# Performance work log

Hardware: AMD Instinct MI355X
Metric: run time of the kernel (lower is better)

The kernel has to match this reference:

```python
import jax, jax.numpy as jnp
import numpy as np

B, S, D, H = 16, 2048, 128, 4
HD = D // H  # 32
EPS = 1e-5


def layer_norm(x, g, b):
    m = jnp.mean(x, axis=-1, keepdims=True)
    v = jnp.mean((x - m) ** 2, axis=-1, keepdims=True)
    return (x - m) * jax.lax.rsqrt(v + EPS) * g + b


def setup_inputs() -> dict:
    key = jax.random.key(0)
    ks = jax.random.split(key, 9)
    lin = lambda k: jax.random.normal(k, (D, D), dtype=jnp.float32) * 0.01  # [in, out]
    return {
        "input0": jax.random.normal(ks[0], (B, S, D), dtype=jnp.float32),
        "Wq": lin(ks[1]), "bq": jnp.zeros((D,), jnp.float32),
        "Wk": lin(ks[2]), "bk": jnp.zeros((D,), jnp.float32),
        "Wv": lin(ks[3]), "bv": jnp.zeros((D,), jnp.float32),
        "Wo": lin(ks[4]), "bo": jnp.zeros((D,), jnp.float32),
        "g1": jnp.ones((D,), jnp.float32), "b1": jnp.zeros((D,), jnp.float32),
        "W1": lin(ks[5]), "bf1": jnp.zeros((D,), jnp.float32),
        "W2": lin(ks[6]), "bf2": jnp.zeros((D,), jnp.float32),
        "g2": jnp.ones((D,), jnp.float32), "b2": jnp.zeros((D,), jnp.float32),
    }


def reference(input0, Wq, bq, Wk, bk, Wv, bv, Wo, bo, g1, b1, W1, bf1, W2, bf2, g2, b2):
    x = input0
    # multi-head attention (self-attention), dropout in eval mode (identity)
    q = (x @ Wq + bq).reshape(B, S, H, HD)
    k = (x @ Wk + bk).reshape(B, S, H, HD)
    v = (x @ Wv + bv).reshape(B, S, H, HD)
    scores = jnp.einsum("bqhd,bkhd->bhqk", q, k) / jnp.sqrt(jnp.float32(HD))
    weights = jax.nn.softmax(scores, axis=-1)
    attn = jnp.einsum("bhqk,bkhd->bqhd", weights, v).reshape(B, S, D)
    attn = attn @ Wo + bo
    attended = layer_norm(attn + x, g1, b1)
    # feed-forward; note residual uses x (not attended), faithful to source
    ff = jax.nn.relu(attended @ W1 + bf1) @ W2 + bf2
    return layer_norm(ff + x, g2, b2)
```

## Files before the change

### kernel.cpp

```cpp
#include <hip/hip_runtime.h>
#include <math.h>

#define NB   16
#define NS   2048
#define ND   128
#define NH   4
#define NHD  32
#define NROWS (NB * NS)

typedef unsigned short u16;
typedef __bf16 bf16x8 __attribute__((ext_vector_type(8)));
typedef float  f32x4  __attribute__((ext_vector_type(4)));
typedef float  f32x16 __attribute__((ext_vector_type(16)));

static __device__ __forceinline__ u16 f2bf(float a) {
    union { __bf16 h; u16 u; } t; t.h = (__bf16)a; return t.u;
}
static __device__ __forceinline__ unsigned int pk2(float a, float b) {
    union { __bf16 h[2]; unsigned int u; } t;
    t.h[0] = (__bf16)a; t.h[1] = (__bf16)b; return t.u;
}

#if __has_builtin(__builtin_amdgcn_exp2f)
#define EXP2(x) __builtin_amdgcn_exp2f(x)
#else
extern "C" __device__ float __ocml_native_exp2_f32(float);
#define EXP2(x) __ocml_native_exp2_f32(x)
#endif

#define QSCALE (0.17677669529663687f * 1.4426950408889634f)

__global__ __launch_bounds__(256) void prep_kernel(
    const float* __restrict__ Wq, const float* __restrict__ Wk,
    const float* __restrict__ Wv, const float* __restrict__ Wo,
    const float* __restrict__ W1, const float* __restrict__ W2,
    u16* __restrict__ wt)
{
    const int wb = blockIdx.x, tid = threadIdx.x;
    const int widx = wb >> 3, sub = wb & 7;
    const float* W = widx == 0 ? Wq : widx == 1 ? Wk : widx == 2 ? Wv
                   : widx == 3 ? Wo : widx == 4 ? W1 : W2;
    const int flat8 = sub * 256 + tid;
    const int n = flat8 >> 4, k0 = (flat8 & 15) * 8;
    float v[8];
    #pragma unroll
    for (int j = 0; j < 8; ++j) v[j] = W[(size_t)(k0 + j) * ND + n];
    int4 o;
    o.x = pk2(v[0], v[1]); o.y = pk2(v[2], v[3]);
    o.z = pk2(v[4], v[5]); o.w = pk2(v[6], v[7]);
    *reinterpret_cast<int4*>(wt + (size_t)widx * 16384 + (size_t)n * ND + k0) = o;
}

__global__ __launch_bounds__(256) void qkv_mfma_kernel(
    const float* __restrict__ x,
    const u16* __restrict__ wtq, const u16* __restrict__ wtk, const u16* __restrict__ wtv,
    const float* __restrict__ bq, const float* __restrict__ bk, const float* __restrict__ bv,
    u16* __restrict__ qo, u16* __restrict__ kfo, u16* __restrict__ vfo)
{
    const int tid = threadIdx.x, lane = tid & 63, w = tid >> 6;
    const int n = lane & 15, c = lane >> 4;
    const int row0 = blockIdx.x * 64;
    const int grow = row0 + w * 16;

    bf16x8 a[4];
    #pragma unroll
    for (int kk = 0; kk < 4; ++kk) {
        const float* xp = x + (size_t)(grow + n) * ND + kk * 32 + c * 8;
        float4 f0 = *reinterpret_cast<const float4*>(xp);
        float4 f1 = *reinterpret_cast<const float4*>(xp + 4);
        union { unsigned int u[4]; bf16x8 v; } t;
        t.u[0] = pk2(f0.x, f0.y); t.u[1] = pk2(f0.z, f0.w);
        t.u[2] = pk2(f1.x, f1.y); t.u[3] = pk2(f1.z, f1.w);
        a[kk] = t.v;
    }

    f32x4 accq[8], acck[8], accv[8];
    #pragma unroll
    for (int nb = 0; nb < 8; ++nb) {
        accq[nb] = f32x4{0.f, 0.f, 0.f, 0.f};
        acck[nb] = f32x4{0.f, 0.f, 0.f, 0.f};
        accv[nb] = f32x4{0.f, 0.f, 0.f, 0.f};
    }

    #pragma unroll
    for (int kk = 0; kk < 4; ++kk) {
        #pragma unroll
        for (int nb = 0; nb < 8; ++nb) {
            const size_t boff = (size_t)(nb * 16 + n) * ND + kk * 32 + c * 8;
            bf16x8 bqf = *reinterpret_cast<const bf16x8*>(wtq + boff);
            bf16x8 bkf = *reinterpret_cast<const bf16x8*>(wtk + boff);
            bf16x8 bvf = *reinterpret_cast<const bf16x8*>(wtv + boff);
            accq[nb] = __builtin_amdgcn_mfma_f32_16x16x32_bf16(a[kk], bqf, accq[nb], 0, 0, 0);
            acck[nb] = __builtin_amdgcn_mfma_f32_16x16x32_bf16(a[kk], bkf, acck[nb], 0, 0, 0);
            accv[nb] = __builtin_amdgcn_mfma_f32_16x16x32_bf16(a[kk], bvf, accv[nb], 0, 0, 0);
        }
    }

    const int b   = row0 >> 11;
    const int sp0 = (row0 & (NS - 1)) + w * 16;

    #pragma unroll
    for (int nb = 0; nb < 8; ++nb) {
        const int col = nb * 16 + n, hh = col >> 5, d32 = col & 31;
        const float bqv = bq[col], bkv = bk[col], bvv = bv[col];
        const size_t kvb = ((size_t)b * NH + hh) * (NS * NHD);

        #pragma unroll
        for (int r = 0; r < 4; ++r)
            qo[kvb + (size_t)(sp0 + 4 * c + r) * NHD + d32] =
                f2bf((accq[nb][r] + bqv) * QSCALE);

        const int s = d32 >> 4, c2 = (d32 >> 3) & 1, j = d32 & 7;
        #pragma unroll
        for (int r = 0; r < 4; ++r) {
            const int key = sp0 + 4 * c + r;
            const int T = key >> 5, l5 = key & 31;
            kfo[kvb + (size_t)(T * 2 + s) * 512 + (size_t)(l5 + 32 * c2) * 8 + j] =
                f2bf(acck[nb][r] + bkv);
        }

        const int lanep = d32 + 32 * (c & 1);
        const int j0    = 4 * (c >> 1);
        float v0 = accv[nb][0] + bvv, v1 = accv[nb][1] + bvv;
        float v2 = accv[nb][2] + bvv, v3 = accv[nb][3] + bvv;
        *reinterpret_cast<uint2*>(
            vfo + kvb + (size_t)(sp0 >> 4) * 512 + (size_t)lanep * 8 + j0) =
            make_uint2(pk2(v0, v1), pk2(v2, v3));
    }
}

__global__ __launch_bounds__(256) void attn_mfma_kernel(
    const u16* __restrict__ qg,
    const u16* __restrict__ kfg,
    const u16* __restrict__ vfg,
    u16* __restrict__ ao)
{
    __shared__ float Ol[2][64][17];
    __shared__ float Dl[2][64];

    const int tid = threadIdx.x, lane = tid & 63, w = tid >> 6;
    const int qhalf = w >> 1, khalf = w & 1;
    const int bh = blockIdx.y, b = bh >> 2, h = bh & 3;
    const int n = lane & 31, hf = lane >> 5;
    const size_t fbase = (size_t)bh * (NS * NHD);
    const int q0w = blockIdx.x * 64 + qhalf * 32;

    const bf16x8 qf0 = *reinterpret_cast<const bf16x8*>(
        qg + fbase + (size_t)(q0w + n) * NHD + 8 * hf);
    const bf16x8 qf1 = *reinterpret_cast<const bf16x8*>(
        qg + fbase + (size_t)(q0w + n) * NHD + 16 + 8 * hf);

    f32x16 ot, zz;
    #pragma unroll
    for (int i = 0; i < 16; ++i) { ot[i] = 0.f; zz[i] = 0.f; }
    float lp = 0.f;

    const u16* kf = kfg + fbase + (size_t)lane * 8 + (size_t)khalf * (16 * 4) * 512;
    const u16* vf = vfg + fbase + (size_t)lane * 8 + (size_t)khalf * (16 * 4) * 512;

    for (int t = 0; t < 16; ++t) {
        const bf16x8 ka00 = *reinterpret_cast<const bf16x8*>(kf + (size_t)(4 * t + 0) * 512);
        const bf16x8 ka01 = *reinterpret_cast<const bf16x8*>(kf + (size_t)(4 * t + 1) * 512);
        const bf16x8 ka10 = *reinterpret_cast<const bf16x8*>(kf + (size_t)(4 * t + 2) * 512);
        const bf16x8 ka11 = *reinterpret_cast<const bf16x8*>(kf + (size_t)(4 * t + 3) * 512);
        const bf16x8 va0  = *reinterpret_cast<const bf16x8*>(vf + (size_t)(4 * t + 0) * 512);
        const bf16x8 va1  = *reinterpret_cast<const bf16x8*>(vf + (size_t)(4 * t + 1) * 512);
        const bf16x8 va2  = *reinterpret_cast<const bf16x8*>(vf + (size_t)(4 * t + 2) * 512);
        const bf16x8 va3  = *reinterpret_cast<const bf16x8*>(vf + (size_t)(4 * t + 3) * 512);

        f32x16 s0 = __builtin_amdgcn_mfma_f32_32x32x16_bf16(ka00, qf0, zz, 0, 0, 0);
        s0 = __builtin_amdgcn_mfma_f32_32x32x16_bf16(ka01, qf1, s0, 0, 0, 0);
        f32x16 s1 = __builtin_amdgcn_mfma_f32_32x32x16_bf16(ka10, qf0, zz, 0, 0, 0);
        s1 = __builtin_amdgcn_mfma_f32_32x32x16_bf16(ka11, qf1, s1, 0, 0, 0);

        {
            float p[16];
            #pragma unroll
            for (int r = 0; r < 16; ++r) p[r] = EXP2(s0[r]);
            float t0 = (p[0] + p[1]) + (p[2] + p[3]);
            float t1 = (p[4] + p[5]) + (p[6] + p[7]);
            float t2 = (p[8] + p[9]) + (p[10] + p[11]);
            float t3 = (p[12] + p[13]) + (p[14] + p[15]);
            lp += (t0 + t1) + (t2 + t3);
            union { unsigned int u[4]; bf16x8 v; } pw0, pw1;
            #pragma unroll
            for (int i = 0; i < 4; ++i) pw0.u[i] = pk2(p[2 * i], p[2 * i + 1]);
            #pragma unroll
            for (int i = 0; i < 4; ++i) pw1.u[i] = pk2(p[8 + 2 * i], p[9 + 2 * i]);
            ot = __builtin_amdgcn_mfma_f32_32x32x16_bf16(va0, pw0.v, ot, 0, 0, 0);
            ot = __builtin_amdgcn_mfma_f32_32x32x16_bf16(va1, pw1.v, ot, 0, 0, 0);
        }
        {
            float p[16];
            #pragma unroll
            for (int r = 0; r < 16; ++r) p[r] = EXP2(s1[r]);
            float t0 = (p[0] + p[1]) + (p[2] + p[3]);
            float t1 = (p[4] + p[5]) + (p[6] + p[7]);
            float t2 = (p[8] + p[9]) + (p[10] + p[11]);
            float t3 = (p[12] + p[13]) + (p[14] + p[15]);
            lp += (t0 + t1) + (t2 + t3);
            union { unsigned int u[4]; bf16x8 v; } pw0, pw1;
            #pragma unroll
            for (int i = 0; i < 4; ++i) pw0.u[i] = pk2(p[2 * i], p[2 * i + 1]);
            #pragma unroll
            for (int i = 0; i < 4; ++i) pw1.u[i] = pk2(p[8 + 2 * i], p[9 + 2 * i]);
            ot = __builtin_amdgcn_mfma_f32_32x32x16_bf16(va2, pw0.v, ot, 0, 0, 0);
            ot = __builtin_amdgcn_mfma_f32_32x32x16_bf16(va3, pw1.v, ot, 0, 0, 0);
        }
    }

    float lpt = lp + __shfl_xor(lp, 32);

    if (khalf) {
        #pragma unroll
        for (int i = 0; i < 16; ++i) Ol[qhalf][lane][i] = ot[i];
        Dl[qhalf][lane] = lpt;
    }
    __syncthreads();
    if (!khalf) {
        #pragma unroll
        for (int i = 0; i < 16; ++i) ot[i] += Ol[qhalf][lane][i];
        const float dn  = lpt + Dl[qhalf][lane];
        const float inv = 1.0f / dn;

        u16* orow = ao + ((size_t)b * NS + q0w + n) * ND + h * NHD + 4 * hf;
        #pragma unroll
        for (int g = 0; g < 4; ++g) {
            uint2 wv = make_uint2(pk2(ot[4 * g] * inv, ot[4 * g + 1] * inv),
                                  pk2(ot[4 * g + 2] * inv, ot[4 * g + 3] * inv));
            *reinterpret_cast<uint2*>(orow + 8 * g) = wv;
        }
    }
}

__global__ __launch_bounds__(256) void tail_kernel(
    const u16* __restrict__ A0, const u16* __restrict__ wto,
    const u16* __restrict__ wt1, const u16* __restrict__ wt2,
    const float* __restrict__ bo, const float* __restrict__ bf1,
    const float* __restrict__ bf2, const float* __restrict__ x,
    const float* __restrict__ g1, const float* __restrict__ b1,
    const float* __restrict__ g2, const float* __restrict__ b2,
    float* __restrict__ outp)
{
    __shared__ __align__(16) u16 tile[64][136];
    const int tid = threadIdx.x, lane = tid & 63, w = tid >> 6;
    const int n = lane & 15, c = lane >> 4;
    const int row0 = blockIdx.x * 64;
    const int grow = row0 + w * 16;
    const int lrow = w * 16;

    bf16x8 a[4];
    f32x4 acc[8];

    #pragma unroll
    for (int kk = 0; kk < 4; ++kk)
        a[kk] = *reinterpret_cast<const bf16x8*>(
            A0 + (size_t)(grow + n) * ND + kk * 32 + c * 8);
    #pragma unroll
    for (int nb = 0; nb < 8; ++nb) acc[nb] = f32x4{0.f, 0.f, 0.f, 0.f};
    #pragma unroll
    for (int kk = 0; kk < 4; ++kk)
        #pragma unroll
        for (int nb = 0; nb < 8; ++nb) {
            bf16x8 bw = *reinterpret_cast<const bf16x8*>(
                wto + (size_t)(nb * 16 + n) * ND + kk * 32 + c * 8);
            acc[nb] = __builtin_amdgcn_mfma_f32_16x16x32_bf16(a[kk], bw, acc[nb], 0, 0, 0);
        }

    {
        float vals[8][4];
        float sr[4]  = {0.f, 0.f, 0.f, 0.f};
        float sr2[4] = {0.f, 0.f, 0.f, 0.f};
        #pragma unroll
        for (int nb = 0; nb < 8; ++nb) {
            const int col = nb * 16 + n;
            const float bb = bo[col];
            #pragma unroll
            for (int r = 0; r < 4; ++r) {
                float vv = acc[nb][r] + bb +
                           x[(size_t)(grow + 4 * c + r) * ND + col];
                vals[nb][r] = vv;
                sr[r]  += vv;
                sr2[r] += vv * vv;
            }
        }
        #pragma unroll
        for (int m = 1; m < 16; m <<= 1)
            #pragma unroll
            for (int r = 0; r < 4; ++r) {
                sr[r]  += __shfl_xor(sr[r],  m);
                sr2[r] += __shfl_xor(sr2[r], m);
            }
        #pragma unroll
        for (int r = 0; r < 4; ++r) {
            float mean = sr[r] * (1.f / 128.f);
            float var  = fmaf(-mean, mean, sr2[r] * (1.f / 128.f));
            float rstd = rsqrtf(var + 1e-5f);
            #pragma unroll
            for (int nb = 0; nb < 8; ++nb) {
                const int col = nb * 16 + n;
                float y = fmaf((vals[nb][r] - mean) * rstd, g1[col], b1[col]);
                tile[lrow + 4 * c + r][col] = f2bf(y);
            }
        }
    }
    __syncthreads();

    #pragma unroll
    for (int kk = 0; kk < 4; ++kk)
        a[kk] = *reinterpret_cast<const bf16x8*>(&tile[lrow + n][kk * 32 + c * 8]);
    __syncthreads();
    #pragma unroll
    for (int nb = 0; nb < 8; ++nb) acc[nb] = f32x4{0.f, 0.f, 0.f, 0.f};
    #pragma unroll
    for (int kk = 0; kk < 4; ++kk)
        #pragma unroll
        for (int nb = 0; nb < 8; ++nb) {
            bf16x8 bw = *reinterpret_cast<const bf16x8*>(
                wt1 + (size_t)(nb * 16 + n) * ND + kk * 32 + c * 8);
            acc[nb] = __builtin_amdgcn_mfma_f32_16x16x32_bf16(a[kk], bw, acc[nb], 0, 0, 0);
        }
    #pragma unroll
    for (int nb = 0; nb < 8; ++nb) {
        const int col = nb * 16 + n;
        const float bb = bf1[col];
        #pragma unroll
        for (int r = 0; r < 4; ++r)
            tile[lrow + 4 * c + r][col] = f2bf(fmaxf(acc[nb][r] + bb, 0.f));
    }
    __syncthreads();

    #pragma unroll
    for (int kk = 0; kk < 4; ++kk)
        a[kk] = *reinterpret_cast<const bf16x8*>(&tile[lrow + n][kk * 32 + c * 8]);
    #pragma unroll
    for (int nb = 0; nb < 8; ++nb) acc[nb] = f32x4{0.f, 0.f, 0.f, 0.f};
    #pragma unroll
    for (int kk = 0; kk < 4; ++kk)
        #pragma unroll
        for (int nb = 0; nb < 8; ++nb) {
            bf16x8 bw = *reinterpret_cast<const bf16x8*>(
                wt2 + (size_t)(nb * 16 + n) * ND + kk * 32 + c * 8);
            acc[nb] = __builtin_amdgcn_mfma_f32_16x16x32_bf16(a[kk], bw, acc[nb], 0, 0, 0);
        }
    {
        float vals[8][4];
        float sr[4]  = {0.f, 0.f, 0.f, 0.f};
        float sr2[4] = {0.f, 0.f, 0.f, 0.f};
        #pragma unroll
        for (int nb = 0; nb < 8; ++nb) {
            const int col = nb * 16 + n;
            const float bb = bf2[col];
            #pragma unroll
            for (int r = 0; r < 4; ++r) {
                float vv = acc[nb][r] + bb +
                           x[(size_t)(grow + 4 * c + r) * ND + col];
                vals[nb][r] = vv;
                sr[r]  += vv;
                sr2[r] += vv * vv;
            }
        }
        #pragma unroll
        for (int m = 1; m < 16; m <<= 1)
            #pragma unroll
            for (int r = 0; r < 4; ++r) {
                sr[r]  += __shfl_xor(sr[r],  m);
                sr2[r] += __shfl_xor(sr2[r], m);
            }
        #pragma unroll
        for (int r = 0; r < 4; ++r) {
            float mean = sr[r] * (1.f / 128.f);
            float var  = fmaf(-mean, mean, sr2[r] * (1.f / 128.f));
            float rstd = rsqrtf(var + 1e-5f);
            #pragma unroll
            for (int nb = 0; nb < 8; ++nb) {
                const int col = nb * 16 + n;
                float y = fmaf((vals[nb][r] - mean) * rstd, g2[col], b2[col]);
                outp[(size_t)(grow + 4 * c + r) * ND + col] = y;
            }
        }
    }
}

extern "C" void kernel_launch(void* const* d_in, const int* in_sizes, int n_in,
                              void* d_out, int out_size, void* d_ws, size_t ws_size,
                              hipStream_t stream)
{
    const float* x   = (const float*)d_in[0];
    const float* Wq  = (const float*)d_in[1];
    const float* bq  = (const float*)d_in[2];
    const float* Wk  = (const float*)d_in[3];
    const float* bk  = (const float*)d_in[4];
    const float* Wv  = (const float*)d_in[5];
    const float* bv  = (const float*)d_in[6];
    const float* Wo  = (const float*)d_in[7];
    const float* bo  = (const float*)d_in[8];
    const float* g1  = (const float*)d_in[9];
    const float* b1  = (const float*)d_in[10];
    const float* W1  = (const float*)d_in[11];
    const float* bf1 = (const float*)d_in[12];
    const float* W2  = (const float*)d_in[13];
    const float* bf2 = (const float*)d_in[14];
    const float* g2  = (const float*)d_in[15];
    const float* b2  = (const float*)d_in[16];
    float* outp = (float*)d_out;

    const size_t NE = (size_t)NROWS * ND;
    u16* wt  = (u16*)d_ws;
    u16* qb  = wt + 6 * 16384;
    u16* kfb = qb + NE;
    u16* vfb = kfb + NE;
    u16* aob = vfb + NE;

    dim3 blk(256);
    prep_kernel<<<dim3(48), blk, 0, stream>>>(Wq, Wk, Wv, Wo, W1, W2, wt);
    qkv_mfma_kernel<<<dim3(NROWS / 64), blk, 0, stream>>>(
        x, wt + 0 * 16384, wt + 1 * 16384, wt + 2 * 16384, bq, bk, bv, qb, kfb, vfb);
    attn_mfma_kernel<<<dim3(NS / 64, NB * NH), blk, 0, stream>>>(qb, kfb, vfb, aob);
    tail_kernel<<<dim3(NROWS / 64), blk, 0, stream>>>(
        aob, wt + 3 * 16384, wt + 4 * 16384, wt + 5 * 16384,
        bo, bf1, bf2, x, g1, b1, g2, b2, outp);
}
```

Baseline: 129.6 us.

## Stage K through LDS, transpose Q layout, and software-pipeline attention loop

The QKV kernel now writes Q in a d-major (transposed) layout with packed 8-byte stores. K is staged through a shared-memory tile so it can be written to its fragment layout with 16-byte stores instead of scattered 2-byte stores. The attention kernel uses a 1D grid with a block-id swizzle that groups batch-heads, and restructures the key loop into 32 single-tile iterations that prefetch the next K/V fragments and raise wave priority around the MFMAs. Costs include strided 2-byte gathers to load Q in attention, an extra barrier in the QKV kernel, and a changed L2 access order.

```diff
diff --git a/kernel.cpp b/kernel.cpp
--- a/kernel.cpp
+++ b/kernel.cpp
@@ -55,8 +55,10 @@
     const float* __restrict__ x,
     const u16* __restrict__ wtq, const u16* __restrict__ wtk, const u16* __restrict__ wtv,
     const float* __restrict__ bq, const float* __restrict__ bk, const float* __restrict__ bv,
-    u16* __restrict__ qo, u16* __restrict__ kfo, u16* __restrict__ vfo)
+    u16* __restrict__ qdm, u16* __restrict__ kfo, u16* __restrict__ vfo)
 {
+    __shared__ __align__(16) u16 tileK[64][136];
+
     const int tid = threadIdx.x, lane = tid & 63, w = tid >> 6;
     const int n = lane & 15, c = lane >> 4;
     const int row0 = blockIdx.x * 64;
@@ -96,8 +98,9 @@
         }
     }
 
-    const int b   = row0 >> 11;
-    const int sp0 = (row0 & (NS - 1)) + w * 16;
+    const int b    = row0 >> 11;
+    const int sp0b = row0 & (NS - 1);
+    const int sp0  = sp0b + w * 16;
 
     #pragma unroll
     for (int nb = 0; nb < 8; ++nb) {
@@ -105,19 +108,16 @@
         const float bqv = bq[col], bkv = bk[col], bvv = bv[col];
         const size_t kvb = ((size_t)b * NH + hh) * (NS * NHD);
 
+        float q0 = (accq[nb][0] + bqv) * QSCALE;
+        float q1 = (accq[nb][1] + bqv) * QSCALE;
+        float q2 = (accq[nb][2] + bqv) * QSCALE;
+        float q3 = (accq[nb][3] + bqv) * QSCALE;
+        *reinterpret_cast<uint2*>(qdm + kvb + (size_t)d32 * NS + sp0 + 4 * c) =
+            make_uint2(pk2(q0, q1), pk2(q2, q3));
+
         #pragma unroll
         for (int r = 0; r < 4; ++r)
-            qo[kvb + (size_t)(sp0 + 4 * c + r) * NHD + d32] =
-                f2bf((accq[nb][r] + bqv) * QSCALE);
-
-        const int s = d32 >> 4, c2 = (d32 >> 3) & 1, j = d32 & 7;
-        #pragma unroll
-        for (int r = 0; r < 4; ++r) {
-            const int key = sp0 + 4 * c + r;
-            const int T = key >> 5, l5 = key & 31;
-            kfo[kvb + (size_t)(T * 2 + s) * 512 + (size_t)(l5 + 32 * c2) * 8 + j] =
-                f2bf(acck[nb][r] + bkv);
-        }
+            tileK[w * 16 + 4 * c + r][col] = f2bf(acck[nb][r] + bkv);
 
         const int lanep = d32 + 32 * (c & 1);
         const int j0    = 4 * (c >> 1);
@@ -127,10 +127,29 @@
             vfo + kvb + (size_t)(sp0 >> 4) * 512 + (size_t)lanep * 8 + j0) =
             make_uint2(pk2(v0, v1), pk2(v2, v3));
     }
+
+    __syncthreads();
+
+    {
+        const int lk = w * 16 + (lane >> 2);
+        const int gk = sp0b + lk;
+        const int T = gk >> 5, l5 = gk & 31;
+        #pragma unroll
+        for (int i = 0; i < 4; ++i) {
+            const int m16  = (lane & 3) + 4 * i;
+            const int col0 = m16 * 8;
+            const int hh = col0 >> 5, d32 = col0 & 31;
+            const int s = d32 >> 4, c2 = (d32 >> 3) & 1;
+            const size_t kvb = ((size_t)b * NH + hh) * (NS * NHD);
+            int4 vv = *reinterpret_cast<const int4*>(&tileK[lk][col0]);
+            *reinterpret_cast<int4*>(
+                kfo + kvb + (size_t)(T * 2 + s) * 512 + (size_t)(l5 + 32 * c2) * 8) = vv;
+        }
+    }
 }
 
 __global__ __launch_bounds__(256) void attn_mfma_kernel(
-    const u16* __restrict__ qg,
+    const u16* __restrict__ qdm,
     const u16* __restrict__ kfg,
     const u16* __restrict__ vfg,
     u16* __restrict__ ao)
@@ -140,75 +159,71 @@
 
     const int tid = threadIdx.x, lane = tid & 63, w = tid >> 6;
     const int qhalf = w >> 1, khalf = w & 1;
-    const int bh = blockIdx.y, b = bh >> 2, h = bh & 3;
+
+    const int bid  = blockIdx.x;
+    const int bh   = (bid & 7) * 8 + ((bid >> 3) & 7);
+    const int qblk = bid >> 6;
+    const int b = bh >> 2, h = bh & 3;
     const int n = lane & 31, hf = lane >> 5;
     const size_t fbase = (size_t)bh * (NS * NHD);
-    const int q0w = blockIdx.x * 64 + qhalf * 32;
-
-    const bf16x8 qf0 = *reinterpret_cast<const bf16x8*>(
-        qg + fbase + (size_t)(q0w + n) * NHD + 8 * hf);
-    const bf16x8 qf1 = *reinterpret_cast<const bf16x8*>(
-        qg + fbase + (size_t)(q0w + n) * NHD + 16 + 8 * hf);
+    const int q0w = qblk * 64 + qhalf * 32;
+
+    union { u16 h[8]; bf16x8 v; } q0u, q1u;
+    {
+        const u16* qb = qdm + fbase + (q0w + n);
+        #pragma unroll
+        for (int i = 0; i < 8; ++i) {
+            q0u.h[i] = qb[(size_t)(8 * hf + i) * NS];
+            q1u.h[i] = qb[(size_t)(16 + 8 * hf + i) * NS];
+        }
+    }
+    const bf16x8 qf0 = q0u.v, qf1 = q1u.v;
 
     f32x16 ot, zz;
     #pragma unroll
     for (int i = 0; i < 16; ++i) { ot[i] = 0.f; zz[i] = 0.f; }
-    float lp = 0.f;
-
-    const u16* kf = kfg + fbase + (size_t)lane * 8 + (size_t)khalf * (16 * 4) * 512;
-    const u16* vf = vfg + fbase + (size_t)lane * 8 + (size_t)khalf * (16 * 4) * 512;
-
-    for (int t = 0; t < 16; ++t) {
-        const bf16x8 ka00 = *reinterpret_cast<const bf16x8*>(kf + (size_t)(4 * t + 0) * 512);
-        const bf16x8 ka01 = *reinterpret_cast<const bf16x8*>(kf + (size_t)(4 * t + 1) * 512);
-        const bf16x8 ka10 = *reinterpret_cast<const bf16x8*>(kf + (size_t)(4 * t + 2) * 512);
-        const bf16x8 ka11 = *reinterpret_cast<const bf16x8*>(kf + (size_t)(4 * t + 3) * 512);
-        const bf16x8 va0  = *reinterpret_cast<const bf16x8*>(vf + (size_t)(4 * t + 0) * 512);
-        const bf16x8 va1  = *reinterpret_cast<const bf16x8*>(vf + (size_t)(4 * t + 1) * 512);
-        const bf16x8 va2  = *reinterpret_cast<const bf16x8*>(vf + (size_t)(4 * t + 2) * 512);
-        const bf16x8 va3  = *reinterpret_cast<const bf16x8*>(vf + (size_t)(4 * t + 3) * 512);
-
-        f32x16 s0 = __builtin_amdgcn_mfma_f32_32x32x16_bf16(ka00, qf0, zz, 0, 0, 0);
-        s0 = __builtin_amdgcn_mfma_f32_32x32x16_bf16(ka01, qf1, s0, 0, 0, 0);
-        f32x16 s1 = __builtin_amdgcn_mfma_f32_32x32x16_bf16(ka10, qf0, zz, 0, 0, 0);
-        s1 = __builtin_amdgcn_mfma_f32_32x32x16_bf16(ka11, qf1, s1, 0, 0, 0);
-
-        {
-            float p[16];
-            #pragma unroll
-            for (int r = 0; r < 16; ++r) p[r] = EXP2(s0[r]);
-            float t0 = (p[0] + p[1]) + (p[2] + p[3]);
-            float t1 = (p[4] + p[5]) + (p[6] + p[7]);
-            float t2 = (p[8] + p[9]) + (p[10] + p[11]);
-            float t3 = (p[12] + p[13]) + (p[14] + p[15]);
-            lp += (t0 + t1) + (t2 + t3);
-            union { unsigned int u[4]; bf16x8 v; } pw0, pw1;
-            #pragma unroll
-            for (int i = 0; i < 4; ++i) pw0.u[i] = pk2(p[2 * i], p[2 * i + 1]);
-            #pragma unroll
-            for (int i = 0; i < 4; ++i) pw1.u[i] = pk2(p[8 + 2 * i], p[9 + 2 * i]);
-            ot = __builtin_amdgcn_mfma_f32_32x32x16_bf16(va0, pw0.v, ot, 0, 0, 0);
-            ot = __builtin_amdgcn_mfma_f32_32x32x16_bf16(va1, pw1.v, ot, 0, 0, 0);
-        }
-        {
-            float p[16];
-            #pragma unroll
-            for (int r = 0; r < 16; ++r) p[r] = EXP2(s1[r]);
-            float t0 = (p[0] + p[1]) + (p[2] + p[3]);
-            float t1 = (p[4] + p[5]) + (p[6] + p[7]);
-            float t2 = (p[8] + p[9]) + (p[10] + p[11]);
-            float t3 = (p[12] + p[13]) + (p[14] + p[15]);
-            lp += (t0 + t1) + (t2 + t3);
-            union { unsigned int u[4]; bf16x8 v; } pw0, pw1;
-            #pragma unroll
-            for (int i = 0; i < 4; ++i) pw0.u[i] = pk2(p[2 * i], p[2 * i + 1]);
-            #pragma unroll
-            for (int i = 0; i < 4; ++i) pw1.u[i] = pk2(p[8 + 2 * i], p[9 + 2 * i]);
-            ot = __builtin_amdgcn_mfma_f32_32x32x16_bf16(va2, pw0.v, ot, 0, 0, 0);
-            ot = __builtin_amdgcn_mfma_f32_32x32x16_bf16(va3, pw1.v, ot, 0, 0, 0);
-        }
-    }
-
+    float lp0 = 0.f, lp1 = 0.f;
+
+    const u16* kf = kfg + fbase + (size_t)lane * 8 + (size_t)khalf * 32768;
+    const u16* vf = vfg + fbase + (size_t)lane * 8 + (size_t)khalf * 32768;
+
+    bf16x8 ka0 = *reinterpret_cast<const bf16x8*>(kf);
+    bf16x8 ka1 = *reinterpret_cast<const bf16x8*>(kf + 512);
+    bf16x8 va0 = *reinterpret_cast<const bf16x8*>(vf);
+    bf16x8 va1 = *reinterpret_cast<const bf16x8*>(vf + 512);
+
+    for (int t = 0; t < 32; ++t) {
+        kf += 1024; vf += 1024;
+
+        __builtin_amdgcn_s_setprio(1);
+        f32x16 s = __builtin_amdgcn_mfma_f32_32x32x16_bf16(ka0, qf0, zz, 0, 0, 0);
+        s = __builtin_amdgcn_mfma_f32_32x32x16_bf16(ka1, qf1, s, 0, 0, 0);
+        __builtin_amdgcn_s_setprio(0);
+
+        bf16x8 nka0 = *reinterpret_cast<const bf16x8*>(kf);
+        bf16x8 nka1 = *reinterpret_cast<const bf16x8*>(kf + 512);
+
+        union { unsigned int u[4]; bf16x8 v; } pw0, pw1;
+        #pragma unroll
+        for (int i = 0; i < 8; ++i) {
+            float p0 = EXP2(s[2 * i]);
+            float p1 = EXP2(s[2 * i + 1]);
+            lp0 += p0; lp1 += p1;
+            if (i < 4) pw0.u[i] = pk2(p0, p1);
+            else       pw1.u[i - 4] = pk2(p0, p1);
+        }
+
+        __builtin_amdgcn_s_setprio(1);
+        ot = __builtin_amdgcn_mfma_f32_32x32x16_bf16(va0, pw0.v, ot, 0, 0, 0);
+        ot = __builtin_amdgcn_mfma_f32_32x32x16_bf16(va1, pw1.v, ot, 0, 0, 0);
+        __builtin_amdgcn_s_setprio(0);
+
+        va0 = *reinterpret_cast<const bf16x8*>(vf);
+        va1 = *reinterpret_cast<const bf16x8*>(vf + 512);
+        ka0 = nka0; ka1 = nka1;
+    }
+
+    float lp  = lp0 + lp1;
     float lpt = lp + __shfl_xor(lp, 32);
 
     if (khalf) {
@@ -416,7 +431,7 @@
     prep_kernel<<<dim3(48), blk, 0, stream>>>(Wq, Wk, Wv, Wo, W1, W2, wt);
     qkv_mfma_kernel<<<dim3(NROWS / 64), blk, 0, stream>>>(
         x, wt + 0 * 16384, wt + 1 * 16384, wt + 2 * 16384, bq, bk, bv, qb, kfb, vfb);
-    attn_mfma_kernel<<<dim3(NS / 64, NB * NH), blk, 0, stream>>>(qb, kfb, vfb, aob);
+    attn_mfma_kernel<<<dim3(2048), blk, 0, stream>>>(qb, kfb, vfb, aob);
     tail_kernel<<<dim3(NROWS / 64), blk, 0, stream>>>(
         aob, wt + 3 * 16384, wt + 4 * 16384, wt + 5 * 16384,
         bo, bf1, bf2, x, g1, b1, g2, b2, outp);
```

New measurement: 125.2 us. 3.4% less time.
